# Performance work log

Measured on AMD Instinct MI355X. Metric: run time of the kernel, lower is better.

Reference implementation:

```python
import jax, jax.numpy as jnp
import numpy as np

# ---- static module configuration (mirrors __init__) ----
BIG, SMALL = 13, 3
IN_C = 256
GHOST_RATIO = 0.23
NK = -(-BIG // SMALL)                          # ceil(13/3) = 5 small kernels tile the big one
REP_N = int(IN_C * (1 - GHOST_RATIO)) // 2 * 2 # 196 channels go through the big-kernel path
GHOST_N = IN_C - REP_N                         # 60 identity (ghost) channels
OUT_N = REP_N * NK                             # grouped conv channel-multiplier output
PAD = SMALL - 1                                # conv padding = 2 -> conv output is (H+2, W+2)
CROP = SMALL // 2                              # crop to emulate padding=k//2 on the small axis
MID = BIG // 2
REAL_PAD = [MID - i * SMALL - PAD for i in range(NK)]  # [4, 1, -2, -5, -8] shift offsets
P = BIG                                        # safe zero-pad for static shift slicing
N_PATH = 2
BN_EPS = 1e-5


def _split_indices():
    # exact replication of the module's fixed random ghost/rep channel split
    np.random.seed(123)
    ghost = np.sort(np.random.choice(IN_C, GHOST_N, replace=False))
    rep = np.sort(np.array(list(set(range(IN_C)) - set(ghost.tolist())), dtype=np.int64))
    return jnp.asarray(ghost, jnp.int32), jnp.asarray(rep, jnp.int32)


def _dwconv(x, w):
    # depthwise conv with channel multiplier NK: groups = REP_N
    return jax.lax.conv_general_dilated(
        x, w, window_strides=(1, 1), padding=[(PAD, PAD), (PAD, PAD)],
        dimension_numbers=('NCHW', 'OIHW', 'NCHW'), feature_group_count=REP_N)


def _bn(x, g, b):
    # BatchNorm2d in training mode (batch statistics), matching nn.(Sync)BatchNorm forward
    m = jnp.mean(x, axis=(0, 2, 3), keepdims=True)
    v = jnp.var(x, axis=(0, 2, 3), keepdims=True)
    return (x - m) * jax.lax.rsqrt(v + BN_EPS) * g[None, :, None, None] + b[None, :, None, None]


def setup_inputs() -> dict:
    key = jax.random.key(0)
    ks = jax.random.split(key, 4)
    B, H, W = 32, 56, 56
    inputs = jax.random.normal(ks[0], (B, IN_C, H, W), jnp.float32)
    fan = SMALL * SMALL  # groups=REP_N -> in_ch/groups = 1
    std = (2.0 / fan) ** 0.5
    w1 = jax.random.normal(ks[1], (OUT_N, 1, SMALL, SMALL), jnp.float32) * std
    w2 = jax.random.normal(ks[2], (OUT_N, 1, SMALL, SMALL), jnp.float32) * std
    ghost_idx, rep_idx = _split_indices()
    ones = jnp.ones((REP_N,), jnp.float32)
    zeros = jnp.zeros((REP_N,), jnp.float32)
    return {
        'inputs': inputs, 'w1': w1, 'w2': w2,
        'g1': ones, 'b1': zeros, 'g2': ones, 'b2': zeros, 'g3': ones, 'b3': zeros,
        'ghost_idx': ghost_idx, 'rep_idx': rep_idx,
    }


def reference(inputs, w1, w2, g1, b1, g2, b2, g3, b3, ghost_idx, rep_idx):
    B, C, H, W = inputs.shape
    rep_x = jnp.take(inputs, rep_idx, axis=1)      # [B, REP_N, H, W]
    ghost_x = jnp.take(inputs, ghost_idx, axis=1)  # [B, GHOST_N, H, W]

    # N_path grouped depthwise convs summed (pre-merge branch of the module)
    out = _dwconv(rep_x, w1) + _dwconv(rep_x, w2)  # [B, REP_N*NK, H+2, W+2]
    H2, W2 = out.shape[-2:]
    # grouped conv channel order: channel c -> outputs c*NK .. c*NK+NK-1
    x = out.reshape(B, REP_N, NK, H2, W2)

    # AddShift: stack the NK small-conv responses with shifts to emulate
    # a (BIG x SMALL) kernel (shift along H) and a (SMALL x BIG) kernel (shift along W).
    lora1 = jnp.zeros((B, REP_N, H, W), out.dtype)
    lora2 = jnp.zeros((B, REP_N, H, W), out.dtype)
    for i, r in enumerate(REAL_PAD):  # NK is a small static constant
        ci = x[:, :, i]  # [B, REP_N, H2, W2]
        yh = jnp.pad(ci, ((0, 0), (0, 0), (P, P), (0, 0)))
        lora1 = lora1 + yh[:, :, P - r:P - r + H, CROP:CROP + W]
        yw = jnp.pad(ci, ((0, 0), (0, 0), (0, 0), (P, P)))
        lora2 = lora2 + yw[:, :, CROP:CROP + H, P - r:P - r + W]
    # small-kernel branch: center chunk, cropped to emulate padding=SMALL//2
    small = x[:, :, NK // 2, CROP:CROP + H, CROP:CROP + W]

    y = _bn(lora1, g1, b1) + _bn(lora2, g2, b2) + _bn(small, g3, b3) + rep_x
    return jnp.concatenate([y, ghost_x], axis=1)  # [B, IN_C, H, W]
```

## Files before the change

kernel.cpp:

```cpp
#include <hip/hip_runtime.h>


#define B_    32
#define CIN   256
#define REPN  196
#define HW    56
#define IMG   3136
#define NTOT  (B_ * CIN * IMG)
#define NCONVBLK 1400
#define NGHOSTBLK 1920
#define STASH_ELEMS (B_ * REPN * IMG)

__device__ __forceinline__ void load_row20(float (&w)[20], const float* __restrict__ in,
                                           int base) {
  int i0 = base;      i0 = i0 < 0 ? 0 : i0;
  int i1 = base + 4;  i1 = i1 < 0 ? 0 : i1;
  int i3 = base + 12; i3 = i3 > (NTOT - 4) ? (NTOT - 4) : i3;
  int i4 = base + 16; i4 = i4 > (NTOT - 4) ? (NTOT - 4) : i4;
  const float4 v0 = *reinterpret_cast<const float4*>(in + i0);
  const float4 v1 = *reinterpret_cast<const float4*>(in + i1);
  const float4 v2 = *reinterpret_cast<const float4*>(in + base + 8);
  const float4 v3 = *reinterpret_cast<const float4*>(in + i3);
  const float4 v4 = *reinterpret_cast<const float4*>(in + i4);
  w[0]=v0.x;  w[1]=v0.y;  w[2]=v0.z;  w[3]=v0.w;
  w[4]=v1.x;  w[5]=v1.y;  w[6]=v1.z;  w[7]=v1.w;
  w[8]=v2.x;  w[9]=v2.y;  w[10]=v2.z; w[11]=v2.w;
  w[12]=v3.x; w[13]=v3.y; w[14]=v3.z; w[15]=v3.w;
  w[16]=v4.x; w[17]=v4.y; w[18]=v4.z; w[19]=v4.w;
}

__device__ __forceinline__ unsigned short pack_bf16(float f) {
  unsigned int u = __float_as_uint(f);
  u = u + 0x7FFFu + ((u >> 16) & 1u);
  return (unsigned short)(u >> 16);
}

template <bool STASH>
__launch_bounds__(448)
__global__ void sw_pass1(const float* __restrict__ in, const int* __restrict__ rep_idx,
                         const float* __restrict__ wsum, float* __restrict__ partial,
                         unsigned short* __restrict__ L1, unsigned short* __restrict__ L2,
                         unsigned short* __restrict__ S3) {
  const int bid = blockIdx.x;
  const int tid = threadIdx.x;

  const int c = (bid / 56) * 8 + (bid & 7);
  const int rb = (bid % 56) >> 3;
  if (c >= REPN) return;
  const int h0 = rb * 8;

  const int b = tid / 14;
  const int tw = tid - b * 14;
  const int w0 = tw * 4;
  const int src_c = rep_idx[c];
  const int ibase = (b * CIN + src_c) * IMG;
  const int sbase = (b * REPN + c) * IMG;

  float wv[45];
  #pragma unroll
  for (int j = 0; j < 45; ++j) wv[j] = wsum[c * 45 + j];

  const float ma = (tw >= 2) ? 1.f : 0.f;
  const float mb = (tw >= 1) ? 1.f : 0.f;
  const float mc = (tw <= 12) ? 1.f : 0.f;
  const float md = (tw <= 11) ? 1.f : 0.f;

  float acc1[8][4] = {};
  float acc2[3][4] = {};
  float acc3[3][4] = {};
  float s1 = 0, q1 = 0, s2 = 0, q2 = 0, s3 = 0, q3 = 0;

  #pragma unroll
  for (int s = 0; s < 22; ++s) {
    const int r = h0 - 6 + s;
    if (r >= 0 && r < HW) {
      float win[20];
      load_row20(win, in, ibase + r * HW + w0 - 8);
      #pragma unroll
      for (int e = 0; e < 4; ++e) win[e] *= ma;
      #pragma unroll
      for (int e = 4; e < 8; ++e) win[e] *= mb;
      #pragma unroll
      for (int e = 12; e < 16; ++e) win[e] *= mc;
      #pragma unroll
      for (int e = 16; e < 20; ++e) win[e] *= md;

      #pragma unroll
      for (int lr = 0; lr < 8; ++lr) {
        const int t = s - lr;
        if (t >= 0 && t < 15) {
          #pragma unroll
          for (int kw = 0; kw < 3; ++kw) {
            const float wgt = wv[3 * t + kw];
            #pragma unroll
            for (int dw = 0; dw < 4; ++dw)
              acc1[lr][dw] = fmaf(win[dw + kw + 7], wgt, acc1[lr][dw]);
          }
        }
      }
      #pragma unroll
      for (int lr = 0; lr < 8; ++lr) {
        const int kh = s - lr - 5;
        if (kh >= 0 && kh < 3) {
          #pragma unroll
          for (int T = 0; T < 15; ++T) {
            const float wgt = wv[(T / 3) * 9 + kh * 3 + (T % 3)];
            #pragma unroll
            for (int dw = 0; dw < 4; ++dw)
              acc2[lr % 3][dw] = fmaf(win[dw + T + 2], wgt, acc2[lr % 3][dw]);
          }
          #pragma unroll
          for (int kw = 0; kw < 3; ++kw) {
            const float wgt = wv[18 + kh * 3 + kw];
            #pragma unroll
            for (int dw = 0; dw < 4; ++dw)
              acc3[lr % 3][dw] = fmaf(win[dw + kw + 7], wgt, acc3[lr % 3][dw]);
          }
        }
      }
    }

    if (s >= 14) {
      const int lr = s - 14;
      #pragma unroll
      for (int dw = 0; dw < 4; ++dw) {
        const float v = acc1[lr][dw];
        s1 += v; q1 = fmaf(v, v, q1);
      }
      if (STASH) {
        ushort4 t;
        t.x = pack_bf16(acc1[lr][0]); t.y = pack_bf16(acc1[lr][1]);
        t.z = pack_bf16(acc1[lr][2]); t.w = pack_bf16(acc1[lr][3]);
        *reinterpret_cast<ushort4*>(L1 + sbase + (h0 + lr) * HW + w0) = t;
      }
    }
    if (s >= 7 && s <= 14) {
      const int lr = s - 7;
      if (STASH) {
        ushort4 t2, t3;
        t2.x = pack_bf16(acc2[lr % 3][0]); t2.y = pack_bf16(acc2[lr % 3][1]);
        t2.z = pack_bf16(acc2[lr % 3][2]); t2.w = pack_bf16(acc2[lr % 3][3]);
        t3.x = pack_bf16(acc3[lr % 3][0]); t3.y = pack_bf16(acc3[lr % 3][1]);
        t3.z = pack_bf16(acc3[lr % 3][2]); t3.w = pack_bf16(acc3[lr % 3][3]);
        *reinterpret_cast<ushort4*>(L2 + sbase + (h0 + lr) * HW + w0) = t2;
        *reinterpret_cast<ushort4*>(S3 + sbase + (h0 + lr) * HW + w0) = t3;
      }
      #pragma unroll
      for (int dw = 0; dw < 4; ++dw) {
        const float v2 = acc2[lr % 3][dw], v3 = acc3[lr % 3][dw];
        s2 += v2; q2 = fmaf(v2, v2, q2);
        s3 += v3; q3 = fmaf(v3, v3, q3);
        acc2[lr % 3][dw] = 0.f;
        acc3[lr % 3][dw] = 0.f;
      }
    }
  }

  __shared__ float red[7][6];
  #pragma unroll
  for (int off = 32; off > 0; off >>= 1) {
    s1 += __shfl_down(s1, off); q1 += __shfl_down(q1, off);
    s2 += __shfl_down(s2, off); q2 += __shfl_down(q2, off);
    s3 += __shfl_down(s3, off); q3 += __shfl_down(q3, off);
  }
  const int lane = tid & 63, wid = tid >> 6;
  if (lane == 0) {
    red[wid][0] = s1; red[wid][1] = q1; red[wid][2] = s2;
    red[wid][3] = q2; red[wid][4] = s3; red[wid][5] = q3;
  }
  __syncthreads();
  if (tid < 6) {
    float t = 0;
    #pragma unroll
    for (int w = 0; w < 7; ++w) t += red[w][tid];
    partial[(c * 7 + rb) * 6 + tid] = t;
  }
}

__launch_bounds__(448)
__global__ void sw_pass2r(const float* __restrict__ in, const int* __restrict__ rep_idx,
                          const int* __restrict__ ghost_idx, const float* __restrict__ wsum,
                          const float* __restrict__ stats2, float* __restrict__ out) {
  const int bid = blockIdx.x;
  const int tid = threadIdx.x;

  if (bid >= NCONVBLK) {
    const int g = bid - NCONVBLK;
    const int j = g >> 5, b = g & 31;
    const int src_c = ghost_idx[j];
    const float4* s = reinterpret_cast<const float4*>(in + (size_t)(b * CIN + src_c) * IMG);
    float4* d = reinterpret_cast<float4*>(out + ((size_t)(b * CIN) + REPN + j) * IMG);
    #pragma unroll 1
    for (int i = tid; i < 784; i += 448) d[i] = s[i];
    return;
  }

  const int c = (bid / 56) * 8 + (bid & 7);
  const int rb = (bid % 56) >> 3;
  if (c >= REPN) return;
  const int h0 = rb * 8;

  const int b = tid / 14;
  const int tw = tid - b * 14;
  const int w0 = tw * 4;
  const int src_c = rep_idx[c];
  const int ibase = (b * CIN + src_c) * IMG;

  float wv[45];
  #pragma unroll
  for (int j = 0; j < 45; ++j) wv[j] = wsum[c * 45 + j];

  const float A1 = stats2[c * 4 + 0], A2 = stats2[c * 4 + 1];
  const float A3 = stats2[c * 4 + 2], K_ = stats2[c * 4 + 3];

  const float ma = (tw >= 2) ? 1.f : 0.f;
  const float mb = (tw >= 1) ? 1.f : 0.f;
  const float mc = (tw <= 12) ? 1.f : 0.f;
  const float md = (tw <= 11) ? 1.f : 0.f;

  float acc1[8][4] = {};
  float acc2[3][4] = {};
  float acc3[3][4] = {};
  float stash[7][4];

  #pragma unroll
  for (int s = 0; s < 22; ++s) {
    const int r = h0 - 6 + s;
    if (r >= 0 && r < HW) {
      float win[20];
      load_row20(win, in, ibase + r * HW + w0 - 8);
      #pragma unroll
      for (int e = 0; e < 4; ++e) win[e] *= ma;
      #pragma unroll
      for (int e = 4; e < 8; ++e) win[e] *= mb;
      #pragma unroll
      for (int e = 12; e < 16; ++e) win[e] *= mc;
      #pragma unroll
      for (int e = 16; e < 20; ++e) win[e] *= md;

      #pragma unroll
      for (int lr = 0; lr < 8; ++lr) {
        const int t = s - lr;
        if (t >= 0 && t < 15) {
          #pragma unroll
          for (int kw = 0; kw < 3; ++kw) {
            const float wgt = wv[3 * t + kw];
            #pragma unroll
            for (int dw = 0; dw < 4; ++dw)
              acc1[lr][dw] = fmaf(win[dw + kw + 7], wgt, acc1[lr][dw]);
          }
        }
      }
      #pragma unroll
      for (int lr = 0; lr < 8; ++lr) {
        const int kh = s - lr - 5;
        if (kh >= 0 && kh < 3) {
          #pragma unroll
          for (int T = 0; T < 15; ++T) {
            const float wgt = wv[(T / 3) * 9 + kh * 3 + (T % 3)];
            #pragma unroll
            for (int dw = 0; dw < 4; ++dw)
              acc2[lr % 3][dw] = fmaf(win[dw + T + 2], wgt, acc2[lr % 3][dw]);
          }
          #pragma unroll
          for (int kw = 0; kw < 3; ++kw) {
            const float wgt = wv[18 + kh * 3 + kw];
            #pragma unroll
            for (int dw = 0; dw < 4; ++dw)
              acc3[lr % 3][dw] = fmaf(win[dw + kw + 7], wgt, acc3[lr % 3][dw]);
          }
        }
      }
    }

    if (s >= 14) {
      const int lr = s - 14;
      const int hh = h0 + lr;
      const float4 xv = *reinterpret_cast<const float4*>(in + ibase + hh * HW + w0);
      float4 o;
      o.x = fmaf(A1, acc1[lr][0], stash[lr % 7][0] + K_ + xv.x);
      o.y = fmaf(A1, acc1[lr][1], stash[lr % 7][1] + K_ + xv.y);
      o.z = fmaf(A1, acc1[lr][2], stash[lr % 7][2] + K_ + xv.z);
      o.w = fmaf(A1, acc1[lr][3], stash[lr % 7][3] + K_ + xv.w);
      *reinterpret_cast<float4*>(out + (size_t)(b * CIN + c) * IMG + hh * HW + w0) = o;
    }
    if (s >= 7 && s <= 14) {
      const int lr = s - 7;
      #pragma unroll
      for (int dw = 0; dw < 4; ++dw) {
        stash[lr % 7][dw] = fmaf(A2, acc2[lr % 3][dw], A3 * acc3[lr % 3][dw]);
        acc2[lr % 3][dw] = 0.f;
        acc3[lr % 3][dw] = 0.f;
      }
    }
  }
}

__launch_bounds__(256)
__global__ void sw_norm(const float* __restrict__ in, const int* __restrict__ rep_idx,
                        const int* __restrict__ ghost_idx, const float* __restrict__ stats2,
                        const unsigned short* __restrict__ L1,
                        const unsigned short* __restrict__ L2,
                        const unsigned short* __restrict__ S3,
                        float* __restrict__ out) {
  const int bid = blockIdx.x;
  const int tid = threadIdx.x;
  if (bid >= 6272) {
    const int g = bid - 6272;
    const int j = g >> 5, b = g & 31;
    const int src_c = ghost_idx[j];
    const float4* s = reinterpret_cast<const float4*>(in + (size_t)(b * CIN + src_c) * IMG);
    float4* d = reinterpret_cast<float4*>(out + ((size_t)(b * CIN) + REPN + j) * IMG);
    #pragma unroll 1
    for (int i = tid; i < 784; i += 256) d[i] = s[i];
    return;
  }
  const int c = bid >> 5, b = bid & 31;
  const float A1 = stats2[c * 4 + 0], A2 = stats2[c * 4 + 1];
  const float A3 = stats2[c * 4 + 2], K_ = stats2[c * 4 + 3];
  const int xb4 = (b * CIN + rep_idx[c]) * IMG / 4;
  const int ob4 = (b * CIN + c) * IMG / 4;
  const int sb4 = (b * REPN + c) * IMG / 4;
  const float4* xp = reinterpret_cast<const float4*>(in) + xb4;
  float4* op = reinterpret_cast<float4*>(out) + ob4;
  const ushort4* l1p = reinterpret_cast<const ushort4*>(L1) + sb4;
  const ushort4* l2p = reinterpret_cast<const ushort4*>(L2) + sb4;
  const ushort4* s3p = reinterpret_cast<const ushort4*>(S3) + sb4;
  #pragma unroll 1
  for (int g = tid; g < 784; g += 256) {
    const float4 x = xp[g];
    const ushort4 a = l1p[g], d2 = l2p[g], d3 = s3p[g];
    float4 y;
    y.x = fmaf(A1, __uint_as_float((unsigned)a.x << 16),
          fmaf(A2, __uint_as_float((unsigned)d2.x << 16),
          fmaf(A3, __uint_as_float((unsigned)d3.x << 16), K_ + x.x)));
    y.y = fmaf(A1, __uint_as_float((unsigned)a.y << 16),
          fmaf(A2, __uint_as_float((unsigned)d2.y << 16),
          fmaf(A3, __uint_as_float((unsigned)d3.y << 16), K_ + x.y)));
    y.z = fmaf(A1, __uint_as_float((unsigned)a.z << 16),
          fmaf(A2, __uint_as_float((unsigned)d2.z << 16),
          fmaf(A3, __uint_as_float((unsigned)d3.z << 16), K_ + x.z)));
    y.w = fmaf(A1, __uint_as_float((unsigned)a.w << 16),
          fmaf(A2, __uint_as_float((unsigned)d2.w << 16),
          fmaf(A3, __uint_as_float((unsigned)d3.w << 16), K_ + x.w)));
    op[g] = y;
  }
}

extern "C" __global__ void sw_prep(const float* __restrict__ w1, const float* __restrict__ w2,
                                   float* __restrict__ wsum) {
  int i = blockIdx.x * 256 + threadIdx.x;
  if (i < 8820) wsum[i] = w1[i] + w2[i];
}

extern "C" __global__ void sw_reduce(
    const float* __restrict__ partial,
    const float* __restrict__ g1, const float* __restrict__ b1,
    const float* __restrict__ g2, const float* __restrict__ b2,
    const float* __restrict__ g3, const float* __restrict__ b3,
    float* __restrict__ stats2) {
  const int c = blockIdx.x;
  const int tid = threadIdx.x;
  __shared__ float sm[6];
  if (tid < 6) {
    float s = 0;
    #pragma unroll
    for (int rb = 0; rb < 7; ++rb) s += partial[(c * 7 + rb) * 6 + tid];
    sm[tid] = s;
  }
  __syncthreads();
  if (tid == 0) {
    const float N = 100352.f;
    float m1 = sm[0] / N, v1 = sm[1] / N - m1 * m1;
    float m2 = sm[2] / N, v2 = sm[3] / N - m2 * m2;
    float m3 = sm[4] / N, v3 = sm[5] / N - m3 * m3;
    float A1 = g1[c] * rsqrtf(v1 + 1e-5f);
    float A2 = g2[c] * rsqrtf(v2 + 1e-5f);
    float A3 = g3[c] * rsqrtf(v3 + 1e-5f);
    float K = b1[c] + b2[c] + b3[c] - m1 * A1 - m2 * A2 - m3 * A3;
    stats2[c * 4 + 0] = A1; stats2[c * 4 + 1] = A2;
    stats2[c * 4 + 2] = A3; stats2[c * 4 + 3] = K;
  }
}

extern "C" void kernel_launch(void* const* d_in, const int* in_sizes, int n_in,
                              void* d_out, int out_size, void* d_ws, size_t ws_size,
                              hipStream_t stream) {
  const float* in  = (const float*)d_in[0];
  const float* w1  = (const float*)d_in[1];
  const float* w2  = (const float*)d_in[2];
  const float* g1  = (const float*)d_in[3];
  const float* b1  = (const float*)d_in[4];
  const float* g2  = (const float*)d_in[5];
  const float* b2  = (const float*)d_in[6];
  const float* g3  = (const float*)d_in[7];
  const float* b3  = (const float*)d_in[8];
  const int* ghost_idx = (const int*)d_in[9];
  const int* rep_idx   = (const int*)d_in[10];
  float* out = (float*)d_out;
  float* ws  = (float*)d_ws;

  float* wsum    = ws;
  float* stats2  = ws + 8832;
  float* partial = ws + 9728;
  unsigned short* L1 = reinterpret_cast<unsigned short*>((char*)d_ws + (1u << 18));
  unsigned short* L2 = L1 + STASH_ELEMS;
  unsigned short* S3 = L2 + STASH_ELEMS;
  const size_t need = (1u << 18) + 3ull * STASH_ELEMS * sizeof(unsigned short);

  sw_prep<<<35, 256, 0, stream>>>(w1, w2, wsum);
  if (ws_size >= need) {
    sw_pass1<true><<<NCONVBLK, 448, 0, stream>>>(in, rep_idx, wsum, partial, L1, L2, S3);
    sw_reduce<<<196, 64, 0, stream>>>(partial, g1, b1, g2, b2, g3, b3, stats2);
    sw_norm<<<6272 + NGHOSTBLK, 256, 0, stream>>>(in, rep_idx, ghost_idx, stats2,
                                                  L1, L2, S3, out);
  } else {
    sw_pass1<false><<<NCONVBLK, 448, 0, stream>>>(in, rep_idx, wsum, partial, L1, L2, S3);
    sw_reduce<<<196, 64, 0, stream>>>(partial, g1, b1, g2, b2, g3, b3, stats2);
    sw_pass2r<<<NCONVBLK + NGHOSTBLK, 448, 0, stream>>>(in, rep_idx, ghost_idx, wsum,
                                                        stats2, out);
  }
}
```

Measured before the change: 165.8 us.

## Split pass1 across batch halves and pair row loads branch-free

The first conv/statistics pass now launches twice as many 256-thread blocks, each covering 16 batch images instead of 32, so there are more, smaller blocks to spread across compute units. Rows are loaded two at a time with clamped indices and zero masks instead of a boundary branch, so two rows of global loads are in flight together. The per-block partial statistics grow from 7 to 14 slots per channel, and the reduce kernel sums them accordingly. Costs: 32 of the 256 threads in each block sit idle, and the extra in-flight row buffers raise register pressure.

```diff
diff --git a/kernel.cpp b/kernel.cpp
--- a/kernel.cpp
+++ b/kernel.cpp
@@ -7,7 +7,8 @@
 #define HW    56
 #define IMG   3136
 #define NTOT  (B_ * CIN * IMG)
-#define NCONVBLK 1400
+#define NCONV1   2800
+#define NCONV2R  1400
 #define NGHOSTBLK 1920
 #define STASH_ELEMS (B_ * REPN * IMG)
 
@@ -35,8 +36,88 @@
   return (unsigned short)(u >> 16);
 }
 
+#define ROW_COMPUTE(s_, wrow_, rm_)                                          \
+  do {                                                                       \
+    const int s = (s_);                                                      \
+    const float f0 = ma * (rm_), f1 = mb * (rm_), f2 = (rm_),                \
+                f3 = mc * (rm_), f4 = md * (rm_);                            \
+    float win[20];                                                           \
+    win[0]=wrow_[0]*f0;  win[1]=wrow_[1]*f0;  win[2]=wrow_[2]*f0;  win[3]=wrow_[3]*f0; \
+    win[4]=wrow_[4]*f1;  win[5]=wrow_[5]*f1;  win[6]=wrow_[6]*f1;  win[7]=wrow_[7]*f1; \
+    win[8]=wrow_[8]*f2;  win[9]=wrow_[9]*f2;  win[10]=wrow_[10]*f2; win[11]=wrow_[11]*f2; \
+    win[12]=wrow_[12]*f3; win[13]=wrow_[13]*f3; win[14]=wrow_[14]*f3; win[15]=wrow_[15]*f3; \
+    win[16]=wrow_[16]*f4; win[17]=wrow_[17]*f4; win[18]=wrow_[18]*f4; win[19]=wrow_[19]*f4; \
+    _Pragma("unroll")                                                        \
+    for (int lr = 0; lr < 8; ++lr) {                                         \
+      const int t = s - lr;                                                  \
+      if (t >= 0 && t < 15) {                                                \
+        _Pragma("unroll")                                                    \
+        for (int kw = 0; kw < 3; ++kw) {                                     \
+          const float wgt = wv[3 * t + kw];                                  \
+          _Pragma("unroll")                                                  \
+          for (int dw = 0; dw < 4; ++dw)                                     \
+            acc1[lr][dw] = fmaf(win[dw + kw + 7], wgt, acc1[lr][dw]);        \
+        }                                                                    \
+      }                                                                      \
+    }                                                                        \
+    _Pragma("unroll")                                                        \
+    for (int lr = 0; lr < 8; ++lr) {                                         \
+      const int kh = s - lr - 5;                                             \
+      if (kh >= 0 && kh < 3) {                                               \
+        _Pragma("unroll")                                                    \
+        for (int T = 0; T < 15; ++T) {                                       \
+          const float wgt = wv[(T / 3) * 9 + kh * 3 + (T % 3)];              \
+          _Pragma("unroll")                                                  \
+          for (int dw = 0; dw < 4; ++dw)                                     \
+            acc2[lr % 3][dw] = fmaf(win[dw + T + 2], wgt, acc2[lr % 3][dw]); \
+        }                                                                    \
+        _Pragma("unroll")                                                    \
+        for (int kw = 0; kw < 3; ++kw) {                                     \
+          const float wgt = wv[18 + kh * 3 + kw];                            \
+          _Pragma("unroll")                                                  \
+          for (int dw = 0; dw < 4; ++dw)                                     \
+            acc3[lr % 3][dw] = fmaf(win[dw + kw + 7], wgt, acc3[lr % 3][dw]); \
+        }                                                                    \
+      }                                                                      \
+    }                                                                        \
+    if (s >= 14) {                         \
+      const int lr = s - 14;                                                 \
+      _Pragma("unroll")                                                      \
+      for (int dw = 0; dw < 4; ++dw) {                                       \
+        const float v = acc1[lr][dw];                                        \
+        s1 += v; q1 = fmaf(v, v, q1);                                        \
+      }                                                                      \
+      if (STASH) {                                                           \
+        ushort4 t4;                                                          \
+        t4.x = pack_bf16(acc1[lr][0]); t4.y = pack_bf16(acc1[lr][1]);        \
+        t4.z = pack_bf16(acc1[lr][2]); t4.w = pack_bf16(acc1[lr][3]);        \
+        *reinterpret_cast<ushort4*>(L1 + sbase + (h0 + lr) * HW + w0) = t4;  \
+      }                                                                      \
+    }                                                                        \
+    if (s >= 7 && s <= 14) {         \
+      const int lr = s - 7;                                                  \
+      if (STASH) {                                                           \
+        ushort4 t2, t3;                                                      \
+        t2.x = pack_bf16(acc2[lr % 3][0]); t2.y = pack_bf16(acc2[lr % 3][1]); \
+        t2.z = pack_bf16(acc2[lr % 3][2]); t2.w = pack_bf16(acc2[lr % 3][3]); \
+        t3.x = pack_bf16(acc3[lr % 3][0]); t3.y = pack_bf16(acc3[lr % 3][1]); \
+        t3.z = pack_bf16(acc3[lr % 3][2]); t3.w = pack_bf16(acc3[lr % 3][3]); \
+        *reinterpret_cast<ushort4*>(L2 + sbase + (h0 + lr) * HW + w0) = t2;  \
+        *reinterpret_cast<ushort4*>(S3 + sbase + (h0 + lr) * HW + w0) = t3;  \
+      }                                                                      \
+      _Pragma("unroll")                                                      \
+      for (int dw = 0; dw < 4; ++dw) {                                       \
+        const float v2 = acc2[lr % 3][dw], v3 = acc3[lr % 3][dw];            \
+        s2 += v2; q2 = fmaf(v2, v2, q2);                                     \
+        s3 += v3; q3 = fmaf(v3, v3, q3);                                     \
+        acc2[lr % 3][dw] = 0.f;                                              \
+        acc3[lr % 3][dw] = 0.f;                                              \
+      }                                                                      \
+    }                                                                        \
+  } while (0)
+
 template <bool STASH>
-__launch_bounds__(448)
+__launch_bounds__(256)
 __global__ void sw_pass1(const float* __restrict__ in, const int* __restrict__ rep_idx,
                          const float* __restrict__ wsum, float* __restrict__ partial,
                          unsigned short* __restrict__ L1, unsigned short* __restrict__ L2,
@@ -44,119 +125,56 @@
   const int bid = blockIdx.x;
   const int tid = threadIdx.x;
 
-  const int c = (bid / 56) * 8 + (bid & 7);
-  const int rb = (bid % 56) >> 3;
+  const int c = (bid / 112) * 8 + (bid & 7);
+  const int u = (bid % 112) >> 3;
+  const int rb = u >> 1, bh = u & 1;
   if (c >= REPN) return;
   const int h0 = rb * 8;
 
-  const int b = tid / 14;
-  const int tw = tid - b * 14;
+  const int bloc = tid / 14;
+  const int tw = tid - bloc * 14;
   const int w0 = tw * 4;
-  const int src_c = rep_idx[c];
-  const int ibase = (b * CIN + src_c) * IMG;
-  const int sbase = (b * REPN + c) * IMG;
+  const bool act = (bloc < 16);
 
   float wv[45];
   #pragma unroll
   for (int j = 0; j < 45; ++j) wv[j] = wsum[c * 45 + j];
 
-  const float ma = (tw >= 2) ? 1.f : 0.f;
-  const float mb = (tw >= 1) ? 1.f : 0.f;
-  const float mc = (tw <= 12) ? 1.f : 0.f;
-  const float md = (tw <= 11) ? 1.f : 0.f;
-
-  float acc1[8][4] = {};
-  float acc2[3][4] = {};
-  float acc3[3][4] = {};
   float s1 = 0, q1 = 0, s2 = 0, q2 = 0, s3 = 0, q3 = 0;
 
-  #pragma unroll
-  for (int s = 0; s < 22; ++s) {
-    const int r = h0 - 6 + s;
-    if (r >= 0 && r < HW) {
-      float win[20];
-      load_row20(win, in, ibase + r * HW + w0 - 8);
-      #pragma unroll
-      for (int e = 0; e < 4; ++e) win[e] *= ma;
-      #pragma unroll
-      for (int e = 4; e < 8; ++e) win[e] *= mb;
-      #pragma unroll
-      for (int e = 12; e < 16; ++e) win[e] *= mc;
-      #pragma unroll
-      for (int e = 16; e < 20; ++e) win[e] *= md;
-
-      #pragma unroll
-      for (int lr = 0; lr < 8; ++lr) {
-        const int t = s - lr;
-        if (t >= 0 && t < 15) {
-          #pragma unroll
-          for (int kw = 0; kw < 3; ++kw) {
-            const float wgt = wv[3 * t + kw];
-            #pragma unroll
-            for (int dw = 0; dw < 4; ++dw)
-              acc1[lr][dw] = fmaf(win[dw + kw + 7], wgt, acc1[lr][dw]);
-          }
-        }
-      }
-      #pragma unroll
-      for (int lr = 0; lr < 8; ++lr) {
-        const int kh = s - lr - 5;
-        if (kh >= 0 && kh < 3) {
-          #pragma unroll
-          for (int T = 0; T < 15; ++T) {
-            const float wgt = wv[(T / 3) * 9 + kh * 3 + (T % 3)];
-            #pragma unroll
-            for (int dw = 0; dw < 4; ++dw)
-              acc2[lr % 3][dw] = fmaf(win[dw + T + 2], wgt, acc2[lr % 3][dw]);
-          }
-          #pragma unroll
-          for (int kw = 0; kw < 3; ++kw) {
-            const float wgt = wv[18 + kh * 3 + kw];
-            #pragma unroll
-            for (int dw = 0; dw < 4; ++dw)
-              acc3[lr % 3][dw] = fmaf(win[dw + kw + 7], wgt, acc3[lr % 3][dw]);
-          }
-        }
-      }
+  if (act) {
+    const int b = bh * 16 + bloc;
+    const int src_c = rep_idx[c];
+    const int ibase = (b * CIN + src_c) * IMG;
+    const int sbase = (b * REPN + c) * IMG;
+
+    const float ma = (tw >= 2) ? 1.f : 0.f;
+    const float mb = (tw >= 1) ? 1.f : 0.f;
+    const float mc = (tw <= 12) ? 1.f : 0.f;
+    const float md = (tw <= 11) ? 1.f : 0.f;
+
+    float acc1[8][4] = {};
+    float acc2[3][4] = {};
+    float acc3[3][4] = {};
+
+    #pragma unroll
+    for (int sp = 0; sp < 11; ++sp) {
+      const int sA = 2 * sp, sB = 2 * sp + 1;
+      const int rA0 = h0 - 6 + sA, rB0 = h0 - 6 + sB;
+      const float rmA = (rA0 >= 0 && rA0 < HW) ? 1.f : 0.f;
+      const float rmB = (rB0 >= 0 && rB0 < HW) ? 1.f : 0.f;
+      const int rA = rA0 < 0 ? 0 : (rA0 > 55 ? 55 : rA0);
+      const int rB = rB0 < 0 ? 0 : (rB0 > 55 ? 55 : rB0);
+      float wA[20], wB[20];
+      load_row20(wA, in, ibase + rA * HW + w0 - 8);
+      load_row20(wB, in, ibase + rB * HW + w0 - 8);
+
+      ROW_COMPUTE(sA, wA, rmA);
+      ROW_COMPUTE(sB, wB, rmB);
     }
-
-    if (s >= 14) {
-      const int lr = s - 14;
-      #pragma unroll
-      for (int dw = 0; dw < 4; ++dw) {
-        const float v = acc1[lr][dw];
-        s1 += v; q1 = fmaf(v, v, q1);
-      }
-      if (STASH) {
-        ushort4 t;
-        t.x = pack_bf16(acc1[lr][0]); t.y = pack_bf16(acc1[lr][1]);
-        t.z = pack_bf16(acc1[lr][2]); t.w = pack_bf16(acc1[lr][3]);
-        *reinterpret_cast<ushort4*>(L1 + sbase + (h0 + lr) * HW + w0) = t;
-      }
-    }
-    if (s >= 7 && s <= 14) {
-      const int lr = s - 7;
-      if (STASH) {
-        ushort4 t2, t3;
-        t2.x = pack_bf16(acc2[lr % 3][0]); t2.y = pack_bf16(acc2[lr % 3][1]);
-        t2.z = pack_bf16(acc2[lr % 3][2]); t2.w = pack_bf16(acc2[lr % 3][3]);
-        t3.x = pack_bf16(acc3[lr % 3][0]); t3.y = pack_bf16(acc3[lr % 3][1]);
-        t3.z = pack_bf16(acc3[lr % 3][2]); t3.w = pack_bf16(acc3[lr % 3][3]);
-        *reinterpret_cast<ushort4*>(L2 + sbase + (h0 + lr) * HW + w0) = t2;
-        *reinterpret_cast<ushort4*>(S3 + sbase + (h0 + lr) * HW + w0) = t3;
-      }
-      #pragma unroll
-      for (int dw = 0; dw < 4; ++dw) {
-        const float v2 = acc2[lr % 3][dw], v3 = acc3[lr % 3][dw];
-        s2 += v2; q2 = fmaf(v2, v2, q2);
-        s3 += v3; q3 = fmaf(v3, v3, q3);
-        acc2[lr % 3][dw] = 0.f;
-        acc3[lr % 3][dw] = 0.f;
-      }
-    }
-  }
-
-  __shared__ float red[7][6];
+  }
+
+  __shared__ float red[4][6];
   #pragma unroll
   for (int off = 32; off > 0; off >>= 1) {
     s1 += __shfl_down(s1, off); q1 += __shfl_down(q1, off);
@@ -169,12 +187,9 @@
     red[wid][3] = q2; red[wid][4] = s3; red[wid][5] = q3;
   }
   __syncthreads();
-  if (tid < 6) {
-    float t = 0;
-    #pragma unroll
-    for (int w = 0; w < 7; ++w) t += red[w][tid];
-    partial[(c * 7 + rb) * 6 + tid] = t;
-  }
+  if (tid < 6)
+    partial[(c * 14 + u) * 6 + tid] =
+        red[0][tid] + red[1][tid] + red[2][tid] + red[3][tid];
 }
 
 __launch_bounds__(448)
@@ -184,8 +199,8 @@
   const int bid = blockIdx.x;
   const int tid = threadIdx.x;
 
-  if (bid >= NCONVBLK) {
-    const int g = bid - NCONVBLK;
+  if (bid >= NCONV2R) {
+    const int g = bid - NCONV2R;
     const int j = g >> 5, b = g & 31;
     const int src_c = ghost_idx[j];
     const float4* s = reinterpret_cast<const float4*>(in + (size_t)(b * CIN + src_c) * IMG);
@@ -365,7 +380,7 @@
   if (tid < 6) {
     float s = 0;
     #pragma unroll
-    for (int rb = 0; rb < 7; ++rb) s += partial[(c * 7 + rb) * 6 + tid];
+    for (int u = 0; u < 14; ++u) s += partial[(c * 14 + u) * 6 + tid];
     sm[tid] = s;
   }
   __syncthreads();
@@ -410,14 +425,14 @@
 
   sw_prep<<<35, 256, 0, stream>>>(w1, w2, wsum);
   if (ws_size >= need) {
-    sw_pass1<true><<<NCONVBLK, 448, 0, stream>>>(in, rep_idx, wsum, partial, L1, L2, S3);
+    sw_pass1<true><<<NCONV1, 256, 0, stream>>>(in, rep_idx, wsum, partial, L1, L2, S3);
     sw_reduce<<<196, 64, 0, stream>>>(partial, g1, b1, g2, b2, g3, b3, stats2);
     sw_norm<<<6272 + NGHOSTBLK, 256, 0, stream>>>(in, rep_idx, ghost_idx, stats2,
                                                   L1, L2, S3, out);
   } else {
-    sw_pass1<false><<<NCONVBLK, 448, 0, stream>>>(in, rep_idx, wsum, partial, L1, L2, S3);
+    sw_pass1<false><<<NCONV1, 256, 0, stream>>>(in, rep_idx, wsum, partial, L1, L2, S3);
     sw_reduce<<<196, 64, 0, stream>>>(partial, g1, b1, g2, b2, g3, b3, stats2);
-    sw_pass2r<<<NCONVBLK + NGHOSTBLK, 448, 0, stream>>>(in, rep_idx, ghost_idx, wsum,
-                                                        stats2, out);
-  }
-}
+    sw_pass2r<<<NCONV2R + NGHOSTBLK, 448, 0, stream>>>(in, rep_idx, ghost_idx, wsum,
+                                                       stats2, out);
+  }
+}
```

After: 178.9 us. 7.9% more time.

## Split pass1 into single-wave blocks per batch group, drop block-level reduction

Applied to the files above, without the earlier changes.

Pass1 now launches one 64-lane wave per (channel, row-block, batch-group of 4). This replaces the 448-thread blocks, so the LDS reduction and barrier go away and the grid has more, smaller blocks. Rows outside the image are skipped through static bounds per row-block. Partial statistics grow from 7 to 56 per channel, so the reduce kernel does more serial work, and 8 of the 64 lanes sit idle.

```diff
diff --git a/kernel.cpp b/kernel.cpp
--- a/kernel.cpp
+++ b/kernel.cpp
@@ -7,7 +7,8 @@
 #define HW    56
 #define IMG   3136
 #define NTOT  (B_ * CIN * IMG)
-#define NCONVBLK 1400
+#define NCONV1   11200
+#define NCONV2R  1400
 #define NGHOSTBLK 1920
 #define STASH_ELEMS (B_ * REPN * IMG)
 
@@ -36,144 +37,145 @@
 }
 
 template <bool STASH>
-__launch_bounds__(448)
+__launch_bounds__(64)
 __global__ void sw_pass1(const float* __restrict__ in, const int* __restrict__ rep_idx,
                          const float* __restrict__ wsum, float* __restrict__ partial,
                          unsigned short* __restrict__ L1, unsigned short* __restrict__ L2,
                          unsigned short* __restrict__ S3) {
   const int bid = blockIdx.x;
-  const int tid = threadIdx.x;
-
-  const int c = (bid / 56) * 8 + (bid & 7);
-  const int rb = (bid % 56) >> 3;
+  const int lane = threadIdx.x;
+
+  const int c = (bid / 448) * 8 + (bid & 7);
+  const int v = (bid % 448) >> 3;
+  const int rb = v >> 3, bg = v & 7;
   if (c >= REPN) return;
   const int h0 = rb * 8;
 
-  const int b = tid / 14;
-  const int tw = tid - b * 14;
+  const int bloc = lane / 14;
+  const int tw = lane - bloc * 14;
   const int w0 = tw * 4;
-  const int src_c = rep_idx[c];
-  const int ibase = (b * CIN + src_c) * IMG;
-  const int sbase = (b * REPN + c) * IMG;
+  const bool act = (bloc < 4);
 
   float wv[45];
   #pragma unroll
   for (int j = 0; j < 45; ++j) wv[j] = wsum[c * 45 + j];
 
-  const float ma = (tw >= 2) ? 1.f : 0.f;
-  const float mb = (tw >= 1) ? 1.f : 0.f;
-  const float mc = (tw <= 12) ? 1.f : 0.f;
-  const float md = (tw <= 11) ? 1.f : 0.f;
-
-  float acc1[8][4] = {};
-  float acc2[3][4] = {};
-  float acc3[3][4] = {};
   float s1 = 0, q1 = 0, s2 = 0, q2 = 0, s3 = 0, q3 = 0;
 
-  #pragma unroll
-  for (int s = 0; s < 22; ++s) {
-    const int r = h0 - 6 + s;
-    if (r >= 0 && r < HW) {
-      float win[20];
-      load_row20(win, in, ibase + r * HW + w0 - 8);
-      #pragma unroll
-      for (int e = 0; e < 4; ++e) win[e] *= ma;
-      #pragma unroll
-      for (int e = 4; e < 8; ++e) win[e] *= mb;
-      #pragma unroll
-      for (int e = 12; e < 16; ++e) win[e] *= mc;
-      #pragma unroll
-      for (int e = 16; e < 20; ++e) win[e] *= md;
-
-      #pragma unroll
-      for (int lr = 0; lr < 8; ++lr) {
-        const int t = s - lr;
-        if (t >= 0 && t < 15) {
-          #pragma unroll
-          for (int kw = 0; kw < 3; ++kw) {
-            const float wgt = wv[3 * t + kw];
-            #pragma unroll
-            for (int dw = 0; dw < 4; ++dw)
-              acc1[lr][dw] = fmaf(win[dw + kw + 7], wgt, acc1[lr][dw]);
+  if (act) {
+    const int b = bg * 4 + bloc;
+    const int src_c = rep_idx[c];
+    const int ibase = (b * CIN + src_c) * IMG;
+    const int sbase = (b * REPN + c) * IMG;
+
+    const float ma = (tw >= 2) ? 1.f : 0.f;
+    const float mb = (tw >= 1) ? 1.f : 0.f;
+    const float mc = (tw <= 12) ? 1.f : 0.f;
+    const float md = (tw <= 11) ? 1.f : 0.f;
+
+    const int s_lo = (rb == 0) ? 6 : 0;
+    const int s_hi = (rb == 6) ? 13 : 21;
+
+    float acc1[8][4] = {};
+    float acc2[3][4] = {};
+    float acc3[3][4] = {};
+
+    #pragma unroll
+    for (int s = 0; s < 22; ++s) {
+      if (s >= s_lo && s <= s_hi) {
+        const int r = h0 - 6 + s;
+        float win[20];
+        load_row20(win, in, ibase + r * HW + w0 - 8);
+        #pragma unroll
+        for (int e = 0; e < 4; ++e) win[e] *= ma;
+        #pragma unroll
+        for (int e = 4; e < 8; ++e) win[e] *= mb;
+        #pragma unroll
+        for (int e = 12; e < 16; ++e) win[e] *= mc;
+        #pragma unroll
+        for (int e = 16; e < 20; ++e) win[e] *= md;
+
+        #pragma unroll
+        for (int lr = 0; lr < 8; ++lr) {
+          const int t = s - lr;
+          if (t >= 0 && t < 15) {
+            #pragma unroll
+            for (int kw = 0; kw < 3; ++kw) {
+              const float wgt = wv[3 * t + kw];
+              #pragma unroll
+              for (int dw = 0; dw < 4; ++dw)
+                acc1[lr][dw] = fmaf(win[dw + kw + 7], wgt, acc1[lr][dw]);
+            }
           }
         }
-      }
-      #pragma unroll
-      for (int lr = 0; lr < 8; ++lr) {
-        const int kh = s - lr - 5;
-        if (kh >= 0 && kh < 3) {
-          #pragma unroll
-          for (int T = 0; T < 15; ++T) {
-            const float wgt = wv[(T / 3) * 9 + kh * 3 + (T % 3)];
-            #pragma unroll
-            for (int dw = 0; dw < 4; ++dw)
-              acc2[lr % 3][dw] = fmaf(win[dw + T + 2], wgt, acc2[lr % 3][dw]);
+        #pragma unroll
+        for (int lr = 0; lr < 8; ++lr) {
+          const int kh = s - lr - 5;
+          if (kh >= 0 && kh < 3) {
+            #pragma unroll
+            for (int T = 0; T < 15; ++T) {
+              const float wgt = wv[(T / 3) * 9 + kh * 3 + (T % 3)];
+              #pragma unroll
+              for (int dw = 0; dw < 4; ++dw)
+                acc2[lr % 3][dw] = fmaf(win[dw + T + 2], wgt, acc2[lr % 3][dw]);
+            }
+            #pragma unroll
+            for (int kw = 0; kw < 3; ++kw) {
+              const float wgt = wv[18 + kh * 3 + kw];
+              #pragma unroll
+              for (int dw = 0; dw < 4; ++dw)
+                acc3[lr % 3][dw] = fmaf(win[dw + kw + 7], wgt, acc3[lr % 3][dw]);
+            }
           }
-          #pragma unroll
-          for (int kw = 0; kw < 3; ++kw) {
-            const float wgt = wv[18 + kh * 3 + kw];
-            #pragma unroll
-            for (int dw = 0; dw < 4; ++dw)
-              acc3[lr % 3][dw] = fmaf(win[dw + kw + 7], wgt, acc3[lr % 3][dw]);
-          }
+        }
+      }
+
+      if (s >= 14) {
+        const int lr = s - 14;
+        #pragma unroll
+        for (int dw = 0; dw < 4; ++dw) {
+          const float x = acc1[lr][dw];
+          s1 += x; q1 = fmaf(x, x, q1);
+        }
+        if (STASH) {
+          ushort4 t4;
+          t4.x = pack_bf16(acc1[lr][0]); t4.y = pack_bf16(acc1[lr][1]);
+          t4.z = pack_bf16(acc1[lr][2]); t4.w = pack_bf16(acc1[lr][3]);
+          *reinterpret_cast<ushort4*>(L1 + sbase + (h0 + lr) * HW + w0) = t4;
+        }
+      }
+      if (s >= 7 && s <= 14) {
+        const int lr = s - 7;
+        if (STASH) {
+          ushort4 t2, t3;
+          t2.x = pack_bf16(acc2[lr % 3][0]); t2.y = pack_bf16(acc2[lr % 3][1]);
+          t2.z = pack_bf16(acc2[lr % 3][2]); t2.w = pack_bf16(acc2[lr % 3][3]);
+          t3.x = pack_bf16(acc3[lr % 3][0]); t3.y = pack_bf16(acc3[lr % 3][1]);
+          t3.z = pack_bf16(acc3[lr % 3][2]); t3.w = pack_bf16(acc3[lr % 3][3]);
+          *reinterpret_cast<ushort4*>(L2 + sbase + (h0 + lr) * HW + w0) = t2;
+          *reinterpret_cast<ushort4*>(S3 + sbase + (h0 + lr) * HW + w0) = t3;
+        }
+        #pragma unroll
+        for (int dw = 0; dw < 4; ++dw) {
+          const float v2 = acc2[lr % 3][dw], v3 = acc3[lr % 3][dw];
+          s2 += v2; q2 = fmaf(v2, v2, q2);
+          s3 += v3; q3 = fmaf(v3, v3, q3);
+          acc2[lr % 3][dw] = 0.f;
+          acc3[lr % 3][dw] = 0.f;
         }
       }
     }
-
-    if (s >= 14) {
-      const int lr = s - 14;
-      #pragma unroll
-      for (int dw = 0; dw < 4; ++dw) {
-        const float v = acc1[lr][dw];
-        s1 += v; q1 = fmaf(v, v, q1);
-      }
-      if (STASH) {
-        ushort4 t;
-        t.x = pack_bf16(acc1[lr][0]); t.y = pack_bf16(acc1[lr][1]);
-        t.z = pack_bf16(acc1[lr][2]); t.w = pack_bf16(acc1[lr][3]);
-        *reinterpret_cast<ushort4*>(L1 + sbase + (h0 + lr) * HW + w0) = t;
-      }
-    }
-    if (s >= 7 && s <= 14) {
-      const int lr = s - 7;
-      if (STASH) {
-        ushort4 t2, t3;
-        t2.x = pack_bf16(acc2[lr % 3][0]); t2.y = pack_bf16(acc2[lr % 3][1]);
-        t2.z = pack_bf16(acc2[lr % 3][2]); t2.w = pack_bf16(acc2[lr % 3][3]);
-        t3.x = pack_bf16(acc3[lr % 3][0]); t3.y = pack_bf16(acc3[lr % 3][1]);
-        t3.z = pack_bf16(acc3[lr % 3][2]); t3.w = pack_bf16(acc3[lr % 3][3]);
-        *reinterpret_cast<ushort4*>(L2 + sbase + (h0 + lr) * HW + w0) = t2;
-        *reinterpret_cast<ushort4*>(S3 + sbase + (h0 + lr) * HW + w0) = t3;
-      }
-      #pragma unroll
-      for (int dw = 0; dw < 4; ++dw) {
-        const float v2 = acc2[lr % 3][dw], v3 = acc3[lr % 3][dw];
-        s2 += v2; q2 = fmaf(v2, v2, q2);
-        s3 += v3; q3 = fmaf(v3, v3, q3);
-        acc2[lr % 3][dw] = 0.f;
-        acc3[lr % 3][dw] = 0.f;
-      }
-    }
-  }
-
-  __shared__ float red[7][6];
+  }
+
   #pragma unroll
   for (int off = 32; off > 0; off >>= 1) {
     s1 += __shfl_down(s1, off); q1 += __shfl_down(q1, off);
     s2 += __shfl_down(s2, off); q2 += __shfl_down(q2, off);
     s3 += __shfl_down(s3, off); q3 += __shfl_down(q3, off);
   }
-  const int lane = tid & 63, wid = tid >> 6;
   if (lane == 0) {
-    red[wid][0] = s1; red[wid][1] = q1; red[wid][2] = s2;
-    red[wid][3] = q2; red[wid][4] = s3; red[wid][5] = q3;
-  }
-  __syncthreads();
-  if (tid < 6) {
-    float t = 0;
-    #pragma unroll
-    for (int w = 0; w < 7; ++w) t += red[w][tid];
-    partial[(c * 7 + rb) * 6 + tid] = t;
+    float* p = partial + (size_t)(c * 56 + rb * 8 + bg) * 6;
+    p[0] = s1; p[1] = q1; p[2] = s2; p[3] = q2; p[4] = s3; p[5] = q3;
   }
 }
 
@@ -184,8 +186,8 @@
   const int bid = blockIdx.x;
   const int tid = threadIdx.x;
 
-  if (bid >= NCONVBLK) {
-    const int g = bid - NCONVBLK;
+  if (bid >= NCONV2R) {
+    const int g = bid - NCONV2R;
     const int j = g >> 5, b = g & 31;
     const int src_c = ghost_idx[j];
     const float4* s = reinterpret_cast<const float4*>(in + (size_t)(b * CIN + src_c) * IMG);
@@ -364,8 +366,8 @@
   __shared__ float sm[6];
   if (tid < 6) {
     float s = 0;
-    #pragma unroll
-    for (int rb = 0; rb < 7; ++rb) s += partial[(c * 7 + rb) * 6 + tid];
+    #pragma unroll 1
+    for (int u = 0; u < 56; ++u) s += partial[(size_t)(c * 56 + u) * 6 + tid];
     sm[tid] = s;
   }
   __syncthreads();
@@ -403,21 +405,21 @@
   float* wsum    = ws;
   float* stats2  = ws + 8832;
   float* partial = ws + 9728;
-  unsigned short* L1 = reinterpret_cast<unsigned short*>((char*)d_ws + (1u << 18));
+  unsigned short* L1 = reinterpret_cast<unsigned short*>((char*)d_ws + (1u << 19));
   unsigned short* L2 = L1 + STASH_ELEMS;
   unsigned short* S3 = L2 + STASH_ELEMS;
-  const size_t need = (1u << 18) + 3ull * STASH_ELEMS * sizeof(unsigned short);
+  const size_t need = (1u << 19) + 3ull * STASH_ELEMS * sizeof(unsigned short);
 
   sw_prep<<<35, 256, 0, stream>>>(w1, w2, wsum);
   if (ws_size >= need) {
-    sw_pass1<true><<<NCONVBLK, 448, 0, stream>>>(in, rep_idx, wsum, partial, L1, L2, S3);
+    sw_pass1<true><<<NCONV1, 64, 0, stream>>>(in, rep_idx, wsum, partial, L1, L2, S3);
     sw_reduce<<<196, 64, 0, stream>>>(partial, g1, b1, g2, b2, g3, b3, stats2);
     sw_norm<<<6272 + NGHOSTBLK, 256, 0, stream>>>(in, rep_idx, ghost_idx, stats2,
                                                   L1, L2, S3, out);
   } else {
-    sw_pass1<false><<<NCONVBLK, 448, 0, stream>>>(in, rep_idx, wsum, partial, L1, L2, S3);
+    sw_pass1<false><<<NCONV1, 64, 0, stream>>>(in, rep_idx, wsum, partial, L1, L2, S3);
     sw_reduce<<<196, 64, 0, stream>>>(partial, g1, b1, g2, b2, g3, b3, stats2);
-    sw_pass2r<<<NCONVBLK + NGHOSTBLK, 448, 0, stream>>>(in, rep_idx, ghost_idx, wsum,
-                                                        stats2, out);
-  }
-}
+    sw_pass2r<<<NCONV2R + NGHOSTBLK, 448, 0, stream>>>(in, rep_idx, ghost_idx, wsum,
+                                                       stats2, out);
+  }
+}
```

New measurement: 210.4 us. 26.9% more time.

## Process two batch images per thread in pass1 with 256-thread blocks

Applied to the files above, without the earlier changes.

Pass1 now uses 256-thread blocks where 224 active threads each compute two batch images (b and b+16). The same row window offsets and weight registers serve both, so fewer threads issue the weight and index work and each has more independent FMAs. It also skips the out-of-image halo rows through per-block row bounds instead of a per-row check. The cost is roughly double the accumulator registers per thread, which may lower occupancy or cause spills, and 32 idle lanes per block.

```diff
diff --git a/kernel.cpp b/kernel.cpp
--- a/kernel.cpp
+++ b/kernel.cpp
@@ -7,7 +7,8 @@
 #define HW    56
 #define IMG   3136
 #define NTOT  (B_ * CIN * IMG)
-#define NCONVBLK 1400
+#define NCONV1   1400
+#define NCONV2R  1400
 #define NGHOSTBLK 1920
 #define STASH_ELEMS (B_ * REPN * IMG)
 
@@ -36,7 +37,7 @@
 }
 
 template <bool STASH>
-__launch_bounds__(448)
+__launch_bounds__(256)
 __global__ void sw_pass1(const float* __restrict__ in, const int* __restrict__ rep_idx,
                          const float* __restrict__ wsum, float* __restrict__ partial,
                          unsigned short* __restrict__ L1, unsigned short* __restrict__ L2,
@@ -49,114 +50,144 @@
   if (c >= REPN) return;
   const int h0 = rb * 8;
 
-  const int b = tid / 14;
-  const int tw = tid - b * 14;
+  const int bq = tid / 14;
+  const int tw = tid - bq * 14;
   const int w0 = tw * 4;
-  const int src_c = rep_idx[c];
-  const int ibase = (b * CIN + src_c) * IMG;
-  const int sbase = (b * REPN + c) * IMG;
+  const bool act = (bq < 16);
 
   float wv[45];
   #pragma unroll
   for (int j = 0; j < 45; ++j) wv[j] = wsum[c * 45 + j];
 
-  const float ma = (tw >= 2) ? 1.f : 0.f;
-  const float mb = (tw >= 1) ? 1.f : 0.f;
-  const float mc = (tw <= 12) ? 1.f : 0.f;
-  const float md = (tw <= 11) ? 1.f : 0.f;
-
-  float acc1[8][4] = {};
-  float acc2[3][4] = {};
-  float acc3[3][4] = {};
   float s1 = 0, q1 = 0, s2 = 0, q2 = 0, s3 = 0, q3 = 0;
 
-  #pragma unroll
-  for (int s = 0; s < 22; ++s) {
-    const int r = h0 - 6 + s;
-    if (r >= 0 && r < HW) {
-      float win[20];
-      load_row20(win, in, ibase + r * HW + w0 - 8);
-      #pragma unroll
-      for (int e = 0; e < 4; ++e) win[e] *= ma;
-      #pragma unroll
-      for (int e = 4; e < 8; ++e) win[e] *= mb;
-      #pragma unroll
-      for (int e = 12; e < 16; ++e) win[e] *= mc;
-      #pragma unroll
-      for (int e = 16; e < 20; ++e) win[e] *= md;
-
-      #pragma unroll
-      for (int lr = 0; lr < 8; ++lr) {
-        const int t = s - lr;
-        if (t >= 0 && t < 15) {
-          #pragma unroll
-          for (int kw = 0; kw < 3; ++kw) {
-            const float wgt = wv[3 * t + kw];
-            #pragma unroll
-            for (int dw = 0; dw < 4; ++dw)
-              acc1[lr][dw] = fmaf(win[dw + kw + 7], wgt, acc1[lr][dw]);
+  if (act) {
+    const int src_c = rep_idx[c];
+    const int ibaseA = (bq * CIN + src_c) * IMG;
+    const int ibaseB = ((bq + 16) * CIN + src_c) * IMG;
+    const int sbaseA = (bq * REPN + c) * IMG;
+    const int sbaseB = ((bq + 16) * REPN + c) * IMG;
+
+    const float ma = (tw >= 2) ? 1.f : 0.f;
+    const float mb = (tw >= 1) ? 1.f : 0.f;
+    const float mc = (tw <= 12) ? 1.f : 0.f;
+    const float md = (tw <= 11) ? 1.f : 0.f;
+
+    const int s_lo = (rb == 0) ? 6 : 0;
+    const int s_hi = (rb == 6) ? 13 : 21;
+
+    float a1A[8][4] = {}, a1B[8][4] = {};
+    float a2A[3][4] = {}, a2B[3][4] = {};
+    float a3A[3][4] = {}, a3B[3][4] = {};
+
+    #pragma unroll
+    for (int s = 0; s < 22; ++s) {
+      if (s >= s_lo && s <= s_hi) {
+        const int r = h0 - 6 + s;
+        const int roff = r * HW + w0 - 8;
+        float wA[20], wB[20];
+        load_row20(wA, in, ibaseA + roff);
+        load_row20(wB, in, ibaseB + roff);
+        #pragma unroll
+        for (int e = 0; e < 4; ++e)  { wA[e] *= ma; wB[e] *= ma; }
+        #pragma unroll
+        for (int e = 4; e < 8; ++e)  { wA[e] *= mb; wB[e] *= mb; }
+        #pragma unroll
+        for (int e = 12; e < 16; ++e) { wA[e] *= mc; wB[e] *= mc; }
+        #pragma unroll
+        for (int e = 16; e < 20; ++e) { wA[e] *= md; wB[e] *= md; }
+
+        #pragma unroll
+        for (int lr = 0; lr < 8; ++lr) {
+          const int t = s - lr;
+          if (t >= 0 && t < 15) {
+            #pragma unroll
+            for (int kw = 0; kw < 3; ++kw) {
+              const float wgt = wv[3 * t + kw];
+              #pragma unroll
+              for (int dw = 0; dw < 4; ++dw) {
+                a1A[lr][dw] = fmaf(wA[dw + kw + 7], wgt, a1A[lr][dw]);
+                a1B[lr][dw] = fmaf(wB[dw + kw + 7], wgt, a1B[lr][dw]);
+              }
+            }
           }
         }
-      }
-      #pragma unroll
-      for (int lr = 0; lr < 8; ++lr) {
-        const int kh = s - lr - 5;
-        if (kh >= 0 && kh < 3) {
-          #pragma unroll
-          for (int T = 0; T < 15; ++T) {
-            const float wgt = wv[(T / 3) * 9 + kh * 3 + (T % 3)];
-            #pragma unroll
-            for (int dw = 0; dw < 4; ++dw)
-              acc2[lr % 3][dw] = fmaf(win[dw + T + 2], wgt, acc2[lr % 3][dw]);
+        #pragma unroll
+        for (int lr = 0; lr < 8; ++lr) {
+          const int kh = s - lr - 5;
+          if (kh >= 0 && kh < 3) {
+            #pragma unroll
+            for (int T = 0; T < 15; ++T) {
+              const float wgt = wv[(T / 3) * 9 + kh * 3 + (T % 3)];
+              #pragma unroll
+              for (int dw = 0; dw < 4; ++dw) {
+                a2A[lr % 3][dw] = fmaf(wA[dw + T + 2], wgt, a2A[lr % 3][dw]);
+                a2B[lr % 3][dw] = fmaf(wB[dw + T + 2], wgt, a2B[lr % 3][dw]);
+              }
+            }
+            #pragma unroll
+            for (int kw = 0; kw < 3; ++kw) {
+              const float wgt = wv[18 + kh * 3 + kw];
+              #pragma unroll
+              for (int dw = 0; dw < 4; ++dw) {
+                a3A[lr % 3][dw] = fmaf(wA[dw + kw + 7], wgt, a3A[lr % 3][dw]);
+                a3B[lr % 3][dw] = fmaf(wB[dw + kw + 7], wgt, a3B[lr % 3][dw]);
+              }
+            }
           }
-          #pragma unroll
-          for (int kw = 0; kw < 3; ++kw) {
-            const float wgt = wv[18 + kh * 3 + kw];
-            #pragma unroll
-            for (int dw = 0; dw < 4; ++dw)
-              acc3[lr % 3][dw] = fmaf(win[dw + kw + 7], wgt, acc3[lr % 3][dw]);
-          }
+        }
+      }
+
+      if (s >= 14) {
+        const int lr = s - 14;
+        #pragma unroll
+        for (int dw = 0; dw < 4; ++dw) {
+          const float xA = a1A[lr][dw], xB = a1B[lr][dw];
+          s1 += xA + xB; q1 = fmaf(xA, xA, q1); q1 = fmaf(xB, xB, q1);
+        }
+        if (STASH) {
+          ushort4 tA, tB;
+          tA.x = pack_bf16(a1A[lr][0]); tA.y = pack_bf16(a1A[lr][1]);
+          tA.z = pack_bf16(a1A[lr][2]); tA.w = pack_bf16(a1A[lr][3]);
+          tB.x = pack_bf16(a1B[lr][0]); tB.y = pack_bf16(a1B[lr][1]);
+          tB.z = pack_bf16(a1B[lr][2]); tB.w = pack_bf16(a1B[lr][3]);
+          const int ro = (h0 + lr) * HW + w0;
+          *reinterpret_cast<ushort4*>(L1 + sbaseA + ro) = tA;
+          *reinterpret_cast<ushort4*>(L1 + sbaseB + ro) = tB;
+        }
+      }
+      if (s >= 7 && s <= 14) {
+        const int lr = s - 7;
+        if (STASH) {
+          ushort4 t2A, t3A, t2B, t3B;
+          t2A.x = pack_bf16(a2A[lr % 3][0]); t2A.y = pack_bf16(a2A[lr % 3][1]);
+          t2A.z = pack_bf16(a2A[lr % 3][2]); t2A.w = pack_bf16(a2A[lr % 3][3]);
+          t3A.x = pack_bf16(a3A[lr % 3][0]); t3A.y = pack_bf16(a3A[lr % 3][1]);
+          t3A.z = pack_bf16(a3A[lr % 3][2]); t3A.w = pack_bf16(a3A[lr % 3][3]);
+          t2B.x = pack_bf16(a2B[lr % 3][0]); t2B.y = pack_bf16(a2B[lr % 3][1]);
+          t2B.z = pack_bf16(a2B[lr % 3][2]); t2B.w = pack_bf16(a2B[lr % 3][3]);
+          t3B.x = pack_bf16(a3B[lr % 3][0]); t3B.y = pack_bf16(a3B[lr % 3][1]);
+          t3B.z = pack_bf16(a3B[lr % 3][2]); t3B.w = pack_bf16(a3B[lr % 3][3]);
+          const int ro = (h0 + lr) * HW + w0;
+          *reinterpret_cast<ushort4*>(L2 + sbaseA + ro) = t2A;
+          *reinterpret_cast<ushort4*>(S3 + sbaseA + ro) = t3A;
+          *reinterpret_cast<ushort4*>(L2 + sbaseB + ro) = t2B;
+          *reinterpret_cast<ushort4*>(S3 + sbaseB + ro) = t3B;
+        }
+        #pragma unroll
+        for (int dw = 0; dw < 4; ++dw) {
+          const float v2A = a2A[lr % 3][dw], v3A = a3A[lr % 3][dw];
+          const float v2B = a2B[lr % 3][dw], v3B = a3B[lr % 3][dw];
+          s2 += v2A + v2B; q2 = fmaf(v2A, v2A, q2); q2 = fmaf(v2B, v2B, q2);
+          s3 += v3A + v3B; q3 = fmaf(v3A, v3A, q3); q3 = fmaf(v3B, v3B, q3);
+          a2A[lr % 3][dw] = 0.f; a2B[lr % 3][dw] = 0.f;
+          a3A[lr % 3][dw] = 0.f; a3B[lr % 3][dw] = 0.f;
         }
       }
     }
-
-    if (s >= 14) {
-      const int lr = s - 14;
-      #pragma unroll
-      for (int dw = 0; dw < 4; ++dw) {
-        const float v = acc1[lr][dw];
-        s1 += v; q1 = fmaf(v, v, q1);
-      }
-      if (STASH) {
-        ushort4 t;
-        t.x = pack_bf16(acc1[lr][0]); t.y = pack_bf16(acc1[lr][1]);
-        t.z = pack_bf16(acc1[lr][2]); t.w = pack_bf16(acc1[lr][3]);
-        *reinterpret_cast<ushort4*>(L1 + sbase + (h0 + lr) * HW + w0) = t;
-      }
-    }
-    if (s >= 7 && s <= 14) {
-      const int lr = s - 7;
-      if (STASH) {
-        ushort4 t2, t3;
-        t2.x = pack_bf16(acc2[lr % 3][0]); t2.y = pack_bf16(acc2[lr % 3][1]);
-        t2.z = pack_bf16(acc2[lr % 3][2]); t2.w = pack_bf16(acc2[lr % 3][3]);
-        t3.x = pack_bf16(acc3[lr % 3][0]); t3.y = pack_bf16(acc3[lr % 3][1]);
-        t3.z = pack_bf16(acc3[lr % 3][2]); t3.w = pack_bf16(acc3[lr % 3][3]);
-        *reinterpret_cast<ushort4*>(L2 + sbase + (h0 + lr) * HW + w0) = t2;
-        *reinterpret_cast<ushort4*>(S3 + sbase + (h0 + lr) * HW + w0) = t3;
-      }
-      #pragma unroll
-      for (int dw = 0; dw < 4; ++dw) {
-        const float v2 = acc2[lr % 3][dw], v3 = acc3[lr % 3][dw];
-        s2 += v2; q2 = fmaf(v2, v2, q2);
-        s3 += v3; q3 = fmaf(v3, v3, q3);
-        acc2[lr % 3][dw] = 0.f;
-        acc3[lr % 3][dw] = 0.f;
-      }
-    }
-  }
-
-  __shared__ float red[7][6];
+  }
+
+  __shared__ float red[4][6];
   #pragma unroll
   for (int off = 32; off > 0; off >>= 1) {
     s1 += __shfl_down(s1, off); q1 += __shfl_down(q1, off);
@@ -169,12 +200,9 @@
     red[wid][3] = q2; red[wid][4] = s3; red[wid][5] = q3;
   }
   __syncthreads();
-  if (tid < 6) {
-    float t = 0;
-    #pragma unroll
-    for (int w = 0; w < 7; ++w) t += red[w][tid];
-    partial[(c * 7 + rb) * 6 + tid] = t;
-  }
+  if (tid < 6)
+    partial[(c * 7 + rb) * 6 + tid] =
+        red[0][tid] + red[1][tid] + red[2][tid] + red[3][tid];
 }
 
 __launch_bounds__(448)
@@ -184,8 +212,8 @@
   const int bid = blockIdx.x;
   const int tid = threadIdx.x;
 
-  if (bid >= NCONVBLK) {
-    const int g = bid - NCONVBLK;
+  if (bid >= NCONV2R) {
+    const int g = bid - NCONV2R;
     const int j = g >> 5, b = g & 31;
     const int src_c = ghost_idx[j];
     const float4* s = reinterpret_cast<const float4*>(in + (size_t)(b * CIN + src_c) * IMG);
@@ -410,14 +438,14 @@
 
   sw_prep<<<35, 256, 0, stream>>>(w1, w2, wsum);
   if (ws_size >= need) {
-    sw_pass1<true><<<NCONVBLK, 448, 0, stream>>>(in, rep_idx, wsum, partial, L1, L2, S3);
+    sw_pass1<true><<<NCONV1, 256, 0, stream>>>(in, rep_idx, wsum, partial, L1, L2, S3);
     sw_reduce<<<196, 64, 0, stream>>>(partial, g1, b1, g2, b2, g3, b3, stats2);
     sw_norm<<<6272 + NGHOSTBLK, 256, 0, stream>>>(in, rep_idx, ghost_idx, stats2,
                                                   L1, L2, S3, out);
   } else {
-    sw_pass1<false><<<NCONVBLK, 448, 0, stream>>>(in, rep_idx, wsum, partial, L1, L2, S3);
+    sw_pass1<false><<<NCONV1, 256, 0, stream>>>(in, rep_idx, wsum, partial, L1, L2, S3);
     sw_reduce<<<196, 64, 0, stream>>>(partial, g1, b1, g2, b2, g3, b3, stats2);
-    sw_pass2r<<<NCONVBLK + NGHOSTBLK, 448, 0, stream>>>(in, rep_idx, ghost_idx, wsum,
-                                                        stats2, out);
-  }
-}
+    sw_pass2r<<<NCONV2R + NGHOSTBLK, 448, 0, stream>>>(in, rep_idx, ghost_idx, wsum,
+                                                       stats2, out);
+  }
+}
```

Result: slower. 195.7 us (+18.0%).
